# Optimization experiments

Measured on AMD Instinct MI355X. Metric: run time of the kernel, lower is better.

The kernel has to match this reference:

```python
import jax, jax.numpy as jnp
import numpy as np

N = 16384
E = 524288
D_IN, D_HID, D_OUT = 3, 16, 16


def setup_inputs() -> dict:
    key = jax.random.key(0)
    ks = jax.random.split(key, 8)
    node_feats = jax.random.normal(ks[0], (N, D_IN), dtype=jnp.float32)
    edge_idx = jax.random.randint(ks[1], (2, E), 0, N, dtype=jnp.int64)
    # GIN MLP params (Linear(3,16) -> ReLU -> Linear(16,16) -> ReLU), train_eps
    s1 = 1.0 / np.sqrt(D_IN)
    s2 = 1.0 / np.sqrt(D_HID)
    W1 = jax.random.uniform(ks[2], (D_IN, D_HID), jnp.float32, -s1, s1)
    b1 = jax.random.uniform(ks[3], (D_HID,), jnp.float32, -s1, s1)
    W2 = jax.random.uniform(ks[4], (D_HID, D_OUT), jnp.float32, -s2, s2)
    b2 = jax.random.uniform(ks[5], (D_OUT,), jnp.float32, -s2, s2)
    eps = jnp.zeros((), dtype=jnp.float32)  # PyG init eps=0, trainable
    return {"node_feats": node_feats, "edge_idx": edge_idx,
            "W1": W1, "b1": b1, "W2": W2, "b2": b2, "eps": eps}


def reference(node_feats, edge_idx, W1, b1, W2, b2, eps):
    src, tgt = edge_idx[0], edge_idx[1]
    # GIN aggregation: sum of neighbor features via scatter-add over edges
    agg = jax.ops.segment_sum(node_feats[src], tgt, num_segments=N)  # [N, D_IN]
    z = (1.0 + eps) * node_feats + agg
    # 2-layer MLP with ReLU after each linear
    h = jax.nn.relu(z @ W1 + b1)
    h = jax.nn.relu(h @ W2 + b2)  # [N, D_OUT]
    # dense pairwise similarity
    edge_feats = h @ h.T  # [N, N]
    return edge_feats
```

## Files before the change

kernel.cpp:

```cpp
#include <hip/hip_runtime.h>

#define N_NODES 16384
#define N_EDGES 524288
#define TILE_I 128
#define TILE_J 256

typedef float f32x4 __attribute__((ext_vector_type(4)));

__global__ void zero_agg_kernel(float* __restrict__ agg) {
    int i = blockIdx.x * blockDim.x + threadIdx.x;
    if (i < N_NODES * 3) agg[i] = 0.0f;
}

__global__ void scatter_kernel(const int* __restrict__ eidx,
                               const float* __restrict__ x,
                               float* __restrict__ agg) {
    int e = blockIdx.x * blockDim.x + threadIdx.x;
    if (e >= N_EDGES) return;
    int s = eidx[e];
    int t = eidx[N_EDGES + e];
    float f0 = x[s * 3 + 0];
    float f1 = x[s * 3 + 1];
    float f2 = x[s * 3 + 2];
    atomicAdd(&agg[t * 3 + 0], f0);
    atomicAdd(&agg[t * 3 + 1], f1);
    atomicAdd(&agg[t * 3 + 2], f2);
}

__global__ void mlp_kernel(const float* __restrict__ x,
                           const float* __restrict__ agg,
                           const float* __restrict__ W1,
                           const float* __restrict__ b1,
                           const float* __restrict__ W2,
                           const float* __restrict__ b2,
                           const float* __restrict__ eps_p,
                           float* __restrict__ h) {
    int n = blockIdx.x * blockDim.x + threadIdx.x;
    if (n >= N_NODES) return;
    float se = 1.0f + eps_p[0];
    float z0 = se * x[n * 3 + 0] + agg[n * 3 + 0];
    float z1 = se * x[n * 3 + 1] + agg[n * 3 + 1];
    float z2 = se * x[n * 3 + 2] + agg[n * 3 + 2];
    float h1[16];
#pragma unroll
    for (int j = 0; j < 16; ++j) {
        float a = b1[j];
        a += z0 * W1[0 * 16 + j];
        a += z1 * W1[1 * 16 + j];
        a += z2 * W1[2 * 16 + j];
        h1[j] = fmaxf(a, 0.0f);
    }
    float4* h4 = (float4*)&h[n * 16];
#pragma unroll
    for (int oq = 0; oq < 4; ++oq) {
        float4 o;
        float* op = (float*)&o;
#pragma unroll
        for (int c = 0; c < 4; ++c) {
            int oo = oq * 4 + c;
            float a = b2[oo];
#pragma unroll
            for (int j = 0; j < 16; ++j) a += h1[j] * W2[j * 16 + oo];
            op[c] = fmaxf(a, 0.0f);
        }
        h4[oq] = o;
    }
}

__global__ __launch_bounds__(512) void pairwise_kernel(const float* __restrict__ h,
                                                       float* __restrict__ out) {
    __shared__ float hi[TILE_I * 16];
    __shared__ float hjT[16][TILE_J];
    const int i0 = blockIdx.y * TILE_I;
    const int j0 = blockIdx.x * TILE_J;
    const int tid = threadIdx.x;

    const float4* h4 = (const float4*)h;
    float4* hi4 = (float4*)hi;
    hi4[tid] = h4[(size_t)i0 * 4 + tid];
#pragma unroll
    for (int k = 0; k < 2; ++k) {
        int idx = tid + k * 512;
        float4 w = h4[(size_t)j0 * 4 + idx];
        int row = idx >> 2, q = idx & 3;
        hjT[q * 4 + 0][row] = w.x;
        hjT[q * 4 + 1][row] = w.y;
        hjT[q * 4 + 2][row] = w.z;
        hjT[q * 4 + 3][row] = w.w;
    }
    __syncthreads();

    const int tx = tid & 63;
    const int ty = tid >> 6;

    f32x4 hj[16];
#pragma unroll
    for (int k = 0; k < 16; ++k) hj[k] = *(const f32x4*)&hjT[k][tx * 4];

    f32x4* out4 = (f32x4*)out;
    const size_t obase = (size_t)(i0 + ty * 16) * (N_NODES / 4) + (size_t)(j0 >> 2) + tx;

#pragma unroll
    for (int r = 0; r < 16; ++r) {
        const f32x4* hir4 = (const f32x4*)&hi[(ty * 16 + r) * 16];
        f32x4 A0 = hir4[0], A1 = hir4[1], A2 = hir4[2], A3 = hir4[3];
        f32x4 acc = A0.x * hj[0];
        acc += A0.y * hj[1];
        acc += A0.z * hj[2];
        acc += A0.w * hj[3];
        acc += A1.x * hj[4];
        acc += A1.y * hj[5];
        acc += A1.z * hj[6];
        acc += A1.w * hj[7];
        acc += A2.x * hj[8];
        acc += A2.y * hj[9];
        acc += A2.z * hj[10];
        acc += A2.w * hj[11];
        acc += A3.x * hj[12];
        acc += A3.y * hj[13];
        acc += A3.z * hj[14];
        acc += A3.w * hj[15];
        out4[obase + (size_t)r * (N_NODES / 4)] = acc;
    }
}

extern "C" void kernel_launch(void* const* d_in, const int* in_sizes, int n_in,
                              void* d_out, int out_size, void* d_ws, size_t ws_size,
                              hipStream_t stream) {
    const float* node_feats = (const float*)d_in[0];
    const int*   edge_idx   = (const int*)d_in[1];
    const float* W1         = (const float*)d_in[2];
    const float* b1         = (const float*)d_in[3];
    const float* W2         = (const float*)d_in[4];
    const float* b2         = (const float*)d_in[5];
    const float* eps        = (const float*)d_in[6];
    float* out = (float*)d_out;

    float* agg = (float*)d_ws;
    float* h   = (float*)((char*)d_ws + 262144);

    zero_agg_kernel<<<(N_NODES * 3 + 255) / 256, 256, 0, stream>>>(agg);
    scatter_kernel<<<N_EDGES / 256, 256, 0, stream>>>(edge_idx, node_feats, agg);
    mlp_kernel<<<N_NODES / 64, 64, 0, stream>>>(node_feats, agg, W1, b1, W2, b2, eps, h);

    dim3 grid(N_NODES / TILE_J, N_NODES / TILE_I);
    pairwise_kernel<<<grid, 512, 0, stream>>>(h, out);
}
```

Measured before the change: 281.3 us.

## Restructure pairwise kernel into row panels looping over column chunks

Each block now owns a 32-row panel of h kept in shared memory and walks over all columns in 2048-wide chunks. Each thread loads its four j-rows straight from global memory into registers, with no shared-memory transpose. The grid drops from 64x128 blocks to 512 blocks, each writing full output rows, which gives longer contiguous write streams and less block-launch overhead. In exchange, every h_j is reloaded from global/L2 by every panel, and a per-chunk __syncthreads is added that is not needed.

```diff
diff --git a/kernel.cpp b/kernel.cpp
--- a/kernel.cpp
+++ b/kernel.cpp
@@ -2,8 +2,8 @@
 
 #define N_NODES 16384
 #define N_EDGES 524288
-#define TILE_I 128
-#define TILE_J 256
+#define PANEL_I 32
+#define CHUNK_J 2048
 
 typedef float f32x4 __attribute__((ext_vector_type(4)));
 
@@ -69,58 +69,61 @@
 
 __global__ __launch_bounds__(512) void pairwise_kernel(const float* __restrict__ h,
                                                        float* __restrict__ out) {
-    __shared__ float hi[TILE_I * 16];
-    __shared__ float hjT[16][TILE_J];
-    const int i0 = blockIdx.y * TILE_I;
-    const int j0 = blockIdx.x * TILE_J;
+    __shared__ float hi[PANEL_I * 16];
+    const int i0 = blockIdx.x * PANEL_I;
     const int tid = threadIdx.x;
+    const int wid = tid >> 6;
+    const int lane = tid & 63;
 
-    const float4* h4 = (const float4*)h;
-    float4* hi4 = (float4*)hi;
-    hi4[tid] = h4[(size_t)i0 * 4 + tid];
-#pragma unroll
-    for (int k = 0; k < 2; ++k) {
-        int idx = tid + k * 512;
-        float4 w = h4[(size_t)j0 * 4 + idx];
-        int row = idx >> 2, q = idx & 3;
-        hjT[q * 4 + 0][row] = w.x;
-        hjT[q * 4 + 1][row] = w.y;
-        hjT[q * 4 + 2][row] = w.z;
-        hjT[q * 4 + 3][row] = w.w;
+    if (tid < PANEL_I * 4) {
+        ((f32x4*)hi)[tid] = ((const f32x4*)h)[(size_t)i0 * 4 + tid];
     }
     __syncthreads();
 
-    const int tx = tid & 63;
-    const int ty = tid >> 6;
+    const f32x4* hg = (const f32x4*)h;
+    f32x4* out4 = (f32x4*)out;
 
-    f32x4 hj[16];
+    for (int c = 0; c < N_NODES / CHUNK_J; ++c) {
+        const int jbase = c * CHUNK_J + wid * 256 + lane * 4;
+
+        f32x4 hj[16];
 #pragma unroll
-    for (int k = 0; k < 16; ++k) hj[k] = *(const f32x4*)&hjT[k][tx * 4];
+        for (int jj = 0; jj < 4; ++jj) {
+            const size_t jb4 = (size_t)(jbase + jj) * 4;
+            f32x4 q0 = hg[jb4 + 0];
+            f32x4 q1 = hg[jb4 + 1];
+            f32x4 q2 = hg[jb4 + 2];
+            f32x4 q3 = hg[jb4 + 3];
+            hj[0][jj]  = q0.x;  hj[1][jj]  = q0.y;  hj[2][jj]  = q0.z;  hj[3][jj]  = q0.w;
+            hj[4][jj]  = q1.x;  hj[5][jj]  = q1.y;  hj[6][jj]  = q1.z;  hj[7][jj]  = q1.w;
+            hj[8][jj]  = q2.x;  hj[9][jj]  = q2.y;  hj[10][jj] = q2.z;  hj[11][jj] = q2.w;
+            hj[12][jj] = q3.x;  hj[13][jj] = q3.y;  hj[14][jj] = q3.z;  hj[15][jj] = q3.w;
+        }
 
-    f32x4* out4 = (f32x4*)out;
-    const size_t obase = (size_t)(i0 + ty * 16) * (N_NODES / 4) + (size_t)(j0 >> 2) + tx;
-
-#pragma unroll
-    for (int r = 0; r < 16; ++r) {
-        const f32x4* hir4 = (const f32x4*)&hi[(ty * 16 + r) * 16];
-        f32x4 A0 = hir4[0], A1 = hir4[1], A2 = hir4[2], A3 = hir4[3];
-        f32x4 acc = A0.x * hj[0];
-        acc += A0.y * hj[1];
-        acc += A0.z * hj[2];
-        acc += A0.w * hj[3];
-        acc += A1.x * hj[4];
-        acc += A1.y * hj[5];
-        acc += A1.z * hj[6];
-        acc += A1.w * hj[7];
-        acc += A2.x * hj[8];
-        acc += A2.y * hj[9];
-        acc += A2.z * hj[10];
-        acc += A2.w * hj[11];
-        acc += A3.x * hj[12];
-        acc += A3.y * hj[13];
-        acc += A3.z * hj[14];
-        acc += A3.w * hj[15];
-        out4[obase + (size_t)r * (N_NODES / 4)] = acc;
+        const size_t ob = (size_t)i0 * (N_NODES / 4) + (size_t)(jbase >> 2);
+#pragma unroll 8
+        for (int r = 0; r < PANEL_I; ++r) {
+            const f32x4* hr = (const f32x4*)&hi[r * 16];
+            f32x4 a0 = hr[0], a1 = hr[1], a2 = hr[2], a3 = hr[3];
+            f32x4 acc = a0.x * hj[0];
+            acc += a0.y * hj[1];
+            acc += a0.z * hj[2];
+            acc += a0.w * hj[3];
+            acc += a1.x * hj[4];
+            acc += a1.y * hj[5];
+            acc += a1.z * hj[6];
+            acc += a1.w * hj[7];
+            acc += a2.x * hj[8];
+            acc += a2.y * hj[9];
+            acc += a2.z * hj[10];
+            acc += a2.w * hj[11];
+            acc += a3.x * hj[12];
+            acc += a3.y * hj[13];
+            acc += a3.z * hj[14];
+            acc += a3.w * hj[15];
+            out4[ob + (size_t)r * (N_NODES / 4)] = acc;
+        }
+        __syncthreads();
     }
 }
 
@@ -143,6 +146,5 @@
     scatter_kernel<<<N_EDGES / 256, 256, 0, stream>>>(edge_idx, node_feats, agg);
     mlp_kernel<<<N_NODES / 64, 64, 0, stream>>>(node_feats, agg, W1, b1, W2, b2, eps, h);
 
-    dim3 grid(N_NODES / TILE_J, N_NODES / TILE_I);
-    pairwise_kernel<<<grid, 512, 0, stream>>>(h, out);
+    pairwise_kernel<<<N_NODES / PANEL_I, 512, 0, stream>>>(h, out);
 }
```

Result: slower. 329.9 us (+17.3%).
